# Optimization experiments

Hardware: AMD Instinct MI355X
Metric: run time of the kernel (lower is better)

The kernel has to match this reference:

```python
import jax, jax.numpy as jnp
import numpy as np

N = 100000      # nodes
E = 1600000     # edges (before self-loops)
F_IN = 16       # num_node_features
HID = 16        # hid
HEADS = 4       # in_head == out_head
B = 64          # num graphs
G = 16          # num_global_features
NEG_SLOPE = 0.2


def gat_conv(x, src, dst, W, a_src, a_dst, b, concat):
    """PyG-style GATConv. x:[N,F], W:[F,H*C], a_src/a_dst:[H,C], b:[H*C] or [C]."""
    n = x.shape[0]
    H, C = a_src.shape
    h = (x @ W).reshape(n, H, C)                       # [N,H,C]
    alpha_s = (h * a_src).sum(-1)                      # [N,H]
    alpha_d = (h * a_dst).sum(-1)                      # [N,H]
    e = jax.nn.leaky_relu(alpha_s[src] + alpha_d[dst], NEG_SLOPE)  # [E',H]
    # segment softmax over destination nodes (stable; max is grad-free)
    m = jax.lax.stop_gradient(jax.ops.segment_max(e, dst, num_segments=n))
    ex = jnp.exp(e - m[dst])
    denom = jax.ops.segment_sum(ex, dst, num_segments=n)
    alpha = ex / (denom[dst] + 1e-16)                  # [E',H]
    out = jax.ops.segment_sum(h[src] * alpha[:, :, None], dst, num_segments=n)  # [N,H,C]
    out = out.reshape(n, H * C) if concat else out.mean(axis=1)
    return out + b


def setup_inputs() -> dict:
    key = jax.random.key(0)
    ks = jax.random.split(key, 24)
    s = 0.1
    inp = {
        "x": jax.random.normal(ks[0], (N, F_IN), jnp.float32),
        "stats": jax.random.normal(ks[1], (B, G), jnp.float32),
        # conv1: F_IN -> HID, heads=HEADS, concat=True
        "W1": jax.random.normal(ks[2], (F_IN, HEADS * HID), jnp.float32) * s,
        "a1s": jax.random.normal(ks[3], (HEADS, HID), jnp.float32) * s,
        "a1d": jax.random.normal(ks[4], (HEADS, HID), jnp.float32) * s,
        "b1": jnp.zeros((HEADS * HID,), jnp.float32),
        # conv2: HID*HEADS -> HID, heads=HEADS, concat=False
        "W2": jax.random.normal(ks[5], (HEADS * HID, HEADS * HID), jnp.float32) * s,
        "a2s": jax.random.normal(ks[6], (HEADS, HID), jnp.float32) * s,
        "a2d": jax.random.normal(ks[7], (HEADS, HID), jnp.float32) * s,
        "b2": jnp.zeros((HID,), jnp.float32),
        # conv3: HID -> HID, heads=HEADS, concat=False
        "W3": jax.random.normal(ks[8], (HID, HEADS * HID), jnp.float32) * s,
        "a3s": jax.random.normal(ks[9], (HEADS, HID), jnp.float32) * s,
        "a3d": jax.random.normal(ks[10], (HEADS, HID), jnp.float32) * s,
        "b3": jnp.zeros((HID,), jnp.float32),
        # MLP head
        "fw1": jax.random.normal(ks[11], (HID + G, 32), jnp.float32) * s,
        "fb1": jnp.zeros((32,), jnp.float32),
        "fw2": jax.random.normal(ks[12], (32, 16), jnp.float32) * s,
        "fb2": jnp.zeros((16,), jnp.float32),
        "fw3": jax.random.normal(ks[13], (16, 1), jnp.float32) * s,
        "fb3": jnp.zeros((1,), jnp.float32),
        "edge_index": jax.random.randint(ks[14], (2, E), 0, N, jnp.int64),
        "batch": jnp.sort(jax.random.randint(ks[15], (N,), 0, B, jnp.int64)),
    }
    return inp


def reference(x, stats, W1, a1s, a1d, b1, W2, a2s, a2d, b2, W3, a3s, a3d, b3,
              fw1, fb1, fw2, fb2, fw3, fb3, edge_index, batch):
    n = x.shape[0]
    loops = jnp.arange(n, dtype=edge_index.dtype)
    src = jnp.concatenate([edge_index[0], loops])  # add_self_loops=True (PyG default)
    dst = jnp.concatenate([edge_index[1], loops])
    h = jax.nn.elu(gat_conv(x, src, dst, W1, a1s, a1d, b1, True))
    h = jax.nn.elu(gat_conv(h, src, dst, W2, a2s, a2d, b2, False))
    h = gat_conv(h, src, dst, W3, a3s, a3d, b3, False)
    nb = stats.shape[0]
    pooled = jax.ops.segment_sum(h, batch, num_segments=nb)
    counts = jax.ops.segment_sum(jnp.ones((n,), h.dtype), batch, num_segments=nb)
    pooled = pooled / jnp.maximum(counts, 1.0)[:, None]   # global_mean_pool
    z = jnp.concatenate([pooled, stats], axis=1)
    z = jax.nn.relu(z @ fw1 + fb1)
    z = jax.nn.relu(z @ fw2 + fb2)
    return z @ fw3 + fb3
```

## Files before the change

kernel.cpp:

```cpp
#include <hip/hip_runtime.h>
#include <hip/hip_bf16.h>
#include <hip/hip_fp16.h>

#define NNODES 100000
#define NEDGES 1600000
#define NB     64
#define NG     16
#define POOL_SLOTS (NB * NG + NB)

#define BKT_SHIFT 7
#define NPB 128
#define NBKT ((NNODES + NPB - 1) / NPB)
#define BCAP 4096
#define SCAT_BLOCKS 256
#define NL1_BLOCKS 2048

typedef float vf2 __attribute__((ext_vector_type(2)));

__device__ __forceinline__ float leaky02(float v) {
    return v > 0.0f ? v : 0.2f * v;
}

__device__ __forceinline__ unsigned char cvt_fp8(float a) {
    int r = __builtin_amdgcn_cvt_pk_fp8_f32(a, a, 0, false);
    return (unsigned char)(r & 0xFF);
}

__device__ __forceinline__ float4 loadQ4(const unsigned char* p) {
    int u = *(const int*)p;
    vf2 lo = __builtin_amdgcn_cvt_pk_f32_fp8(u, false);
    vf2 hi = __builtin_amdgcn_cvt_pk_f32_fp8(u, true);
    return make_float4(lo.x, lo.y, hi.x, hi.y);
}

__device__ __forceinline__ void storeH4(__half* p, float4 v) {
    __half2 a = __floats2half2_rn(v.x, v.y);
    __half2 b = __floats2half2_rn(v.z, v.w);
    uint2 raw;
    raw.x = *reinterpret_cast<unsigned*>(&a);
    raw.y = *reinterpret_cast<unsigned*>(&b);
    *(uint2*)p = raw;
}

template <int FIN>
__device__ __forceinline__ void nl_body_f32(const float* __restrict__ X,
                                            const float* __restrict__ W,
                                            const float* __restrict__ a_s,
                                            const float* __restrict__ a_d,
                                            unsigned char* __restrict__ H,
                                            float* __restrict__ AS,
                                            float* __restrict__ AD, int n,
                                            int wave0, int nwaves, int lane) {
    int head = lane >> 4;
    float w[FIN];
#pragma unroll
    for (int k = 0; k < FIN; ++k) w[k] = W[k * 64 + lane];
    float asl = a_s[lane], adl = a_d[lane];

    for (int i = wave0; i < n; i += nwaves) {
        const float* __restrict__ xr = X + (size_t)i * FIN;
        float acc = 0.0f;
#pragma unroll
        for (int k = 0; k < FIN; ++k) acc += xr[k] * w[k];
        H[(size_t)i * 64 + lane] = cvt_fp8(acc);
        float s1 = acc * asl, s2 = acc * adl;
#pragma unroll
        for (int off = 1; off < 16; off <<= 1) {
            s1 += __shfl_xor(s1, off);
            s2 += __shfl_xor(s2, off);
        }
        if ((lane & 15) == 0) {
            AS[(size_t)i * 4 + head] = s1;
            AD[(size_t)i * 4 + head] = s2;
        }
    }
}

template <int FIN>
__global__ void node_linear3h(const unsigned* __restrict__ X,
                              const float* __restrict__ W,
                              const float* __restrict__ a_s,
                              const float* __restrict__ a_d,
                              unsigned char* __restrict__ H,
                              float* __restrict__ AS,
                              float* __restrict__ AD, int n) {
    int lane = threadIdx.x & 63;
    int head = lane >> 4;
    int wave = __builtin_amdgcn_readfirstlane(
        (int)((blockIdx.x * blockDim.x + threadIdx.x) >> 6));
    int nwaves = (gridDim.x * blockDim.x) >> 6;

    float w[FIN];
#pragma unroll
    for (int k = 0; k < FIN; ++k) w[k] = W[k * 64 + lane];
    float asl = a_s[lane], adl = a_d[lane];

    for (int i = wave; i < n; i += nwaves) {
        const unsigned* __restrict__ xr = X + (size_t)i * (FIN / 2);
        float acc = 0.0f;
#pragma unroll
        for (int k = 0; k < FIN / 2; ++k) {
            unsigned u = xr[k];
            __half2 hh = *reinterpret_cast<const __half2*>(&u);
            float2 f = __half22float2(hh);
            acc += f.x * w[2 * k] + f.y * w[2 * k + 1];
        }
        H[(size_t)i * 64 + lane] = cvt_fp8(acc);
        float s1 = acc * asl, s2 = acc * adl;
#pragma unroll
        for (int off = 1; off < 16; off <<= 1) {
            s1 += __shfl_xor(s1, off);
            s2 += __shfl_xor(s2, off);
        }
        if ((lane & 15) == 0) {
            AS[(size_t)i * 4 + head] = s1;
            AD[(size_t)i * 4 + head] = s2;
        }
    }
}

__global__ void scatter_nl1(const int* __restrict__ src,
                            const int* __restrict__ dst,
                            int* __restrict__ bucketCnt,
                            unsigned int* __restrict__ pairs, int ne,
                            const float* __restrict__ X,
                            const float* __restrict__ W,
                            const float* __restrict__ a_s,
                            const float* __restrict__ a_d,
                            unsigned char* __restrict__ H,
                            float* __restrict__ AS,
                            float* __restrict__ AD, int n) {
    __shared__ int hist[NBKT];
    __shared__ int base[NBKT];
    int tid = threadIdx.x;

    if (blockIdx.x >= SCAT_BLOCKS) {
        int lane = tid & 63;
        int wave = __builtin_amdgcn_readfirstlane(
            (int)(((blockIdx.x - SCAT_BLOCKS) * blockDim.x + tid) >> 6));
        int nwaves = (NL1_BLOCKS * 256) >> 6;
        nl_body_f32<16>(X, W, a_s, a_d, H, AS, AD, n, wave, nwaves, lane);
        return;
    }

    for (int i = tid; i < NBKT; i += 256) hist[i] = 0;
    __syncthreads();

    int chunk = (ne + SCAT_BLOCKS - 1) / SCAT_BLOCKS;
    int beg = blockIdx.x * chunk;
    int end = min(beg + chunk, ne);

    for (int e0 = beg; e0 < end; e0 += 1024) {
        int d[4];
#pragma unroll
        for (int q = 0; q < 4; ++q) {
            int e = e0 + q * 256 + tid;
            d[q] = (e < end) ? __builtin_nontemporal_load(dst + e) : -1;
        }
#pragma unroll
        for (int q = 0; q < 4; ++q)
            if (d[q] >= 0) atomicAdd(&hist[d[q] >> BKT_SHIFT], 1);
    }
    __syncthreads();

    for (int i = tid; i < NBKT; i += 256) {
        int h = hist[i];
        base[i] = h ? atomicAdd(&bucketCnt[i], h) : 0;
        hist[i] = 0;
    }
    __syncthreads();

    for (int e0 = beg; e0 < end; e0 += 1024) {
        int d[4], s[4];
#pragma unroll
        for (int q = 0; q < 4; ++q) {
            int e = e0 + q * 256 + tid;
            d[q] = (e < end) ? __builtin_nontemporal_load(dst + e) : -1;
            s[q] = (e < end) ? __builtin_nontemporal_load(src + e) : 0;
        }
        int r[4], bkt[4];
#pragma unroll
        for (int q = 0; q < 4; ++q) {
            if (d[q] >= 0) {
                bkt[q] = d[q] >> BKT_SHIFT;
                r[q] = base[bkt[q]] + atomicAdd(&hist[bkt[q]], 1);
            }
        }
#pragma unroll
        for (int q = 0; q < 4; ++q) {
            if (d[q] >= 0 && r[q] < BCAP)
                __builtin_nontemporal_store(
                    (unsigned)s[q] | ((unsigned)(d[q] & (NPB - 1)) << 20),
                    pairs + (size_t)bkt[q] * BCAP + r[q]);
        }
    }
}

__global__ void bucket_sort(const unsigned int* __restrict__ pairs,
                            const int* __restrict__ bucketCnt,
                            int* __restrict__ srcs,
                            int* __restrict__ indptr, int n) {
    __shared__ int hist[NPB];
    __shared__ int offl[NPB];
    __shared__ int cur[NPB];
    __shared__ int red[256];
    __shared__ int lsrc[BCAP];
    int bkt = blockIdx.x;
    int t = threadIdx.x;
    int cnt = min(bucketCnt[bkt], BCAP);

    int partial = 0;
    for (int j = t; j < bkt; j += 256) partial += min(bucketCnt[j], BCAP);
    red[t] = partial;
    if (t < NPB) hist[t] = 0;
    __syncthreads();
    for (int s = 128; s > 0; s >>= 1) {
        if (t < s) red[t] += red[t + s];
        __syncthreads();
    }
    int boff = red[0];
    if (bkt == NBKT - 1 && t == 0) indptr[n] = boff + cnt;

    const unsigned int* __restrict__ p = pairs + (size_t)bkt * BCAP;
    unsigned int v[BCAP / 256];
#pragma unroll
    for (int i = 0; i < BCAP / 256; ++i) {
        int e = i * 256 + t;
        v[i] = 0u;
        if (e < cnt) {
            v[i] = __builtin_nontemporal_load(p + e);
            atomicAdd(&hist[v[i] >> 20], 1);
        }
    }
    __syncthreads();
    if (t < NPB) offl[t] = hist[t];
    __syncthreads();
    for (int off = 1; off < NPB; off <<= 1) {
        int x = 0;
        if (t < NPB && t >= off) x = offl[t - off];
        __syncthreads();
        if (t < NPB && t >= off) offl[t] += x;
        __syncthreads();
    }
    if (t < NPB) {
        int ex = offl[t] - hist[t];
        cur[t] = ex;
        int node = bkt * NPB + t;
        if (node < n) indptr[node] = boff + ex;
    }
    __syncthreads();
#pragma unroll
    for (int i = 0; i < BCAP / 256; ++i) {
        int e = i * 256 + t;
        if (e < cnt) {
            int r = atomicAdd(&cur[v[i] >> 20], 1);
            lsrc[r] = (int)(v[i] & 0xFFFFFu);
        }
    }
    __syncthreads();
    for (int e = t; e < cnt; e += 256) srcs[boff + e] = lsrc[e];
}

__device__ __forceinline__ float4 gat_agg_core(
    const unsigned char* __restrict__ H, const float* __restrict__ AS,
    const float* __restrict__ AD,
    const int* __restrict__ indptr, const int* __restrict__ srcs,
    int d, int grp, int sl, int head) {
    int beg = indptr[d], end = indptr[d + 1];
    int myS = 0;
    if (beg < end && sl < min(16, end - beg))
        myS = __builtin_nontemporal_load(srcs + beg + sl);

    float ad  = AD[(size_t)d * 4 + head];
    float asd = AS[(size_t)d * 4 + head];
    float t0 = asd + ad;
    float wself = __expf(leaky02(t0));
    float den = wself;
    float4 h4s = loadQ4(H + (size_t)d * 64 + sl * 4);
    float4 acc = make_float4(wself * h4s.x, wself * h4s.y,
                             wself * h4s.z, wself * h4s.w);

    for (int e0 = beg; e0 < end; e0 += 16) {
        int cnt = min(16, end - e0);
        int j = 0;
        for (; j + 8 <= cnt; j += 8) {
            int s[8]; float a[8]; float4 h4[8];
#pragma unroll
            for (int q = 0; q < 8; ++q)
                s[q] = __shfl(myS, (grp << 4) + j + q);
#pragma unroll
            for (int q = 0; q < 8; ++q)
                a[q] = AS[(size_t)s[q] * 4 + head];
#pragma unroll
            for (int q = 0; q < 8; ++q)
                h4[q] = loadQ4(H + (size_t)s[q] * 64 + sl * 4);
#pragma unroll
            for (int q = 0; q < 8; ++q) {
                float t = a[q] + ad;
                float w = __expf(leaky02(t));
                den += w;
                acc.x += w * h4[q].x; acc.y += w * h4[q].y;
                acc.z += w * h4[q].z; acc.w += w * h4[q].w;
            }
        }
        for (; j + 4 <= cnt; j += 4) {
            int s[4]; float a[4]; float4 h4[4];
#pragma unroll
            for (int q = 0; q < 4; ++q)
                s[q] = __shfl(myS, (grp << 4) + j + q);
#pragma unroll
            for (int q = 0; q < 4; ++q)
                a[q] = AS[(size_t)s[q] * 4 + head];
#pragma unroll
            for (int q = 0; q < 4; ++q)
                h4[q] = loadQ4(H + (size_t)s[q] * 64 + sl * 4);
#pragma unroll
            for (int q = 0; q < 4; ++q) {
                float t = a[q] + ad;
                float w = __expf(leaky02(t));
                den += w;
                acc.x += w * h4[q].x; acc.y += w * h4[q].y;
                acc.z += w * h4[q].z; acc.w += w * h4[q].w;
            }
        }
        for (; j < cnt; ++j) {
            int s = __shfl(myS, (grp << 4) + j);
            float t = AS[(size_t)s * 4 + head] + ad;
            float w = __expf(leaky02(t));
            float4 h4 = loadQ4(H + (size_t)s * 64 + sl * 4);
            den += w;
            acc.x += w * h4.x; acc.y += w * h4.y;
            acc.z += w * h4.z; acc.w += w * h4.w;
        }
        int nb = e0 + 16;
        if (nb < end && sl < min(16, end - nb))
            myS = __builtin_nontemporal_load(srcs + nb + sl);
    }
    float inv = 1.0f / (den + 1e-16f);
    return make_float4(acc.x * inv, acc.y * inv, acc.z * inv, acc.w * inv);
}

__global__ void gat_pull_l1(const unsigned char* __restrict__ H,
                            const float* __restrict__ AS,
                            const float* __restrict__ AD,
                            const int* __restrict__ indptr,
                            const int* __restrict__ srcs,
                            const float* __restrict__ bias,
                            __half* __restrict__ out, int n) {
    int lane = threadIdx.x & 63;
    int grp = lane >> 4, sl = lane & 15, head = sl >> 2;
    int wave = (blockIdx.x * blockDim.x + threadIdx.x) >> 6;
    int nwaves = (gridDim.x * blockDim.x) >> 6;
    for (int d0 = wave * 4; d0 < n; d0 += nwaves * 4) {
        int d = d0 + grp;
        if (d < n) {
            float4 v = gat_agg_core(H, AS, AD, indptr, srcs, d, grp, sl, head);
            float4 b4 = *(const float4*)(bias + sl * 4);
            v.x += b4.x; v.y += b4.y; v.z += b4.z; v.w += b4.w;
            v.x = v.x > 0.f ? v.x : __expf(v.x) - 1.f;
            v.y = v.y > 0.f ? v.y : __expf(v.y) - 1.f;
            v.z = v.z > 0.f ? v.z : __expf(v.z) - 1.f;
            v.w = v.w > 0.f ? v.w : __expf(v.w) - 1.f;
            storeH4(out + (size_t)d * 64 + sl * 4, v);
        }
    }
}

__global__ void gat_pull_l2(const unsigned char* __restrict__ H,
                            const float* __restrict__ AS,
                            float* __restrict__ AD,
                            const int* __restrict__ indptr,
                            const int* __restrict__ srcs,
                            const float* __restrict__ bias,
                            const float* __restrict__ W3,
                            const float* __restrict__ a3s,
                            const float* __restrict__ a3d,
                            unsigned char* __restrict__ Hout,
                            float* __restrict__ ASout, int n) {
    __shared__ float w3s[16 * 64];
    for (int i = threadIdx.x; i < 16 * 64; i += 256) w3s[i] = W3[i];
    __syncthreads();

    int lane = threadIdx.x & 63;
    int grp = lane >> 4, sl = lane & 15, head = sl >> 2;
    int wave = (blockIdx.x * blockDim.x + threadIdx.x) >> 6;
    int nwaves = (gridDim.x * blockDim.x) >> 6;
    float4 as4 = *(const float4*)(a3s + head * 16 + (sl & 3) * 4);
    float4 ad4 = *(const float4*)(a3d + head * 16 + (sl & 3) * 4);
    float4 b4  = *(const float4*)(bias + (sl & 3) * 4);

    for (int d0 = wave * 4; d0 < n; d0 += nwaves * 4) {
        int d = d0 + grp;
        if (d < n) {
            float4 v = gat_agg_core(H, AS, AD, indptr, srcs, d, grp, sl, head);
#pragma unroll
            for (int off = 4; off <= 8; off <<= 1) {
                v.x += __shfl_xor(v.x, off);
                v.y += __shfl_xor(v.y, off);
                v.z += __shfl_xor(v.z, off);
                v.w += __shfl_xor(v.w, off);
            }
            v.x = 0.25f * v.x + b4.x; v.y = 0.25f * v.y + b4.y;
            v.z = 0.25f * v.z + b4.z; v.w = 0.25f * v.w + b4.w;
            v.x = v.x > 0.f ? v.x : __expf(v.x) - 1.f;
            v.y = v.y > 0.f ? v.y : __expf(v.y) - 1.f;
            v.z = v.z > 0.f ? v.z : __expf(v.z) - 1.f;
            v.w = v.w > 0.f ? v.w : __expf(v.w) - 1.f;

            float xin[16];
#pragma unroll
            for (int q = 0; q < 4; ++q) {
                int srcl = (grp << 4) + q;
                xin[4 * q + 0] = __shfl(v.x, srcl);
                xin[4 * q + 1] = __shfl(v.y, srcl);
                xin[4 * q + 2] = __shfl(v.z, srcl);
                xin[4 * q + 3] = __shfl(v.w, srcl);
            }
            float4 o = make_float4(0.f, 0.f, 0.f, 0.f);
#pragma unroll
            for (int k = 0; k < 16; ++k) {
                float4 wr = *(const float4*)&w3s[k * 64 + 4 * sl];
                o.x += xin[k] * wr.x; o.y += xin[k] * wr.y;
                o.z += xin[k] * wr.z; o.w += xin[k] * wr.w;
            }
            int pk = __builtin_amdgcn_cvt_pk_fp8_f32(o.x, o.y, 0, false);
            pk = __builtin_amdgcn_cvt_pk_fp8_f32(o.z, o.w, pk, true);
            *(int*)(Hout + (size_t)d * 64 + 4 * sl) = pk;
            float s1 = o.x * as4.x + o.y * as4.y + o.z * as4.z + o.w * as4.w;
            float s2 = o.x * ad4.x + o.y * ad4.y + o.z * ad4.z + o.w * ad4.w;
            s1 += __shfl_xor(s1, 1); s1 += __shfl_xor(s1, 2);
            s2 += __shfl_xor(s2, 1); s2 += __shfl_xor(s2, 2);
            if ((sl & 3) == 0) {
                ASout[(size_t)d * 4 + head] = s1;
                AD[(size_t)d * 4 + head] = s2;
            }
        }
    }
}

__global__ void gat_pull_l3(const unsigned char* __restrict__ H,
                            const float* __restrict__ AS,
                            const float* __restrict__ AD,
                            const int* __restrict__ indptr,
                            const int* __restrict__ srcs,
                            const float* __restrict__ bias,
                            const int* __restrict__ batch,
                            float* __restrict__ PC, int n) {
    __shared__ float lp[POOL_SLOTS];
    for (int i = threadIdx.x; i < POOL_SLOTS; i += 256) lp[i] = 0.f;
    __syncthreads();

    int lane = threadIdx.x & 63;
    int grp = lane >> 4, sl = lane & 15, head = sl >> 2;
    int wave = (blockIdx.x * blockDim.x + threadIdx.x) >> 6;
    int nwaves = (gridDim.x * blockDim.x) >> 6;
    float4 b4 = *(const float4*)(bias + (sl & 3) * 4);

    for (int d0 = wave * 4; d0 < n; d0 += nwaves * 4) {
        int d = d0 + grp;
        if (d < n) {
            float4 v = gat_agg_core(H, AS, AD, indptr, srcs, d, grp, sl, head);
#pragma unroll
            for (int off = 4; off <= 8; off <<= 1) {
                v.x += __shfl_xor(v.x, off);
                v.y += __shfl_xor(v.y, off);
                v.z += __shfl_xor(v.z, off);
                v.w += __shfl_xor(v.w, off);
            }
            v.x = 0.25f * v.x + b4.x; v.y = 0.25f * v.y + b4.y;
            v.z = 0.25f * v.z + b4.z; v.w = 0.25f * v.w + b4.w;
            if (sl < 4) {
                int b = batch[d];
                atomicAdd(&lp[b * 16 + sl * 4 + 0], v.x);
                atomicAdd(&lp[b * 16 + sl * 4 + 1], v.y);
                atomicAdd(&lp[b * 16 + sl * 4 + 2], v.z);
                atomicAdd(&lp[b * 16 + sl * 4 + 3], v.w);
                if (sl == 0) atomicAdd(&lp[NB * NG + b], 1.0f);
            }
        }
    }
    __syncthreads();
    for (int i = threadIdx.x; i < POOL_SLOTS; i += 256) {
        float s = lp[i];
        if (s != 0.f) atomicAdd(&PC[i], s);
    }
}

__global__ void mlp_head(const float* __restrict__ pooled_counts,
                         const float* __restrict__ stats,
                         const float* __restrict__ fw1, const float* __restrict__ fb1,
                         const float* __restrict__ fw2, const float* __restrict__ fb2,
                         const float* __restrict__ fw3, const float* __restrict__ fb3,
                         float* __restrict__ out) {
    int g = threadIdx.x;
    if (g >= NB) return;
    const float* pooled = pooled_counts;
    const float* counts = pooled_counts + NB * NG;
    float z[32];
    float inv = 1.0f / fmaxf(counts[g], 1.0f);
#pragma unroll
    for (int c = 0; c < 16; ++c) z[c] = pooled[g * 16 + c] * inv;
#pragma unroll
    for (int c = 0; c < 16; ++c) z[16 + c] = stats[g * 16 + c];

    float z1[32];
#pragma unroll
    for (int j = 0; j < 32; ++j) {
        float acc = fb1[j];
        for (int k = 0; k < 32; ++k) acc += z[k] * fw1[k * 32 + j];
        z1[j] = fmaxf(acc, 0.0f);
    }
    float z2[16];
#pragma unroll
    for (int j = 0; j < 16; ++j) {
        float acc = fb2[j];
        for (int k = 0; k < 32; ++k) acc += z1[k] * fw2[k * 16 + j];
        z2[j] = fmaxf(acc, 0.0f);
    }
    float acc = fb3[0];
#pragma unroll
    for (int k = 0; k < 16; ++k) acc += z2[k] * fw3[k];
    out[g] = acc;
}

extern "C" void kernel_launch(void* const* d_in, const int* in_sizes, int n_in,
                              void* d_out, int out_size, void* d_ws, size_t ws_size,
                              hipStream_t stream) {
    const float* x    = (const float*)d_in[0];
    const float* stats= (const float*)d_in[1];
    const float* W1   = (const float*)d_in[2];
    const float* a1s  = (const float*)d_in[3];
    const float* a1d  = (const float*)d_in[4];
    const float* b1   = (const float*)d_in[5];
    const float* W2   = (const float*)d_in[6];
    const float* a2s  = (const float*)d_in[7];
    const float* a2d  = (const float*)d_in[8];
    const float* b2   = (const float*)d_in[9];
    const float* W3   = (const float*)d_in[10];
    const float* a3s  = (const float*)d_in[11];
    const float* a3d  = (const float*)d_in[12];
    const float* b3   = (const float*)d_in[13];
    const float* fw1  = (const float*)d_in[14];
    const float* fb1  = (const float*)d_in[15];
    const float* fw2  = (const float*)d_in[16];
    const float* fb2  = (const float*)d_in[17];
    const float* fw3  = (const float*)d_in[18];
    const float* fb3  = (const float*)d_in[19];
    const int* ei     = (const int*)d_in[20];
    const int* batch  = (const int*)d_in[21];

    const int n = NNODES, ne = NEDGES;
    const int* srcI = ei;
    const int* dstI = ei + ne;

    unsigned char* HqA = (unsigned char*)d_ws;
    unsigned char* HqB = HqA + (size_t)n * 64;
    float* ASa  = (float*)(HqB + (size_t)n * 64);
    float* ASb  = ASa + (size_t)n * 4;
    float* AD   = ASb + (size_t)n * 4;
    float* PC   = AD + (size_t)n * 4;
    int* bucketCnt = (int*)(PC + POOL_SLOTS);
    int* indptr    = bucketCnt + NBKT;
    int* srcs      = indptr + (n + 1);
    size_t off = (size_t)((char*)(srcs + ne) - (char*)d_ws);
    off = (off + 255) & ~(size_t)255;
    unsigned int* pairs = (unsigned int*)((char*)d_ws + off);
    __half* B16 = (__half*)pairs;

    const int TB = 256;
    const int nlBlocks   = 2048;
    const int pullBlocks = (n + 15) / 16;

    hipMemsetAsync(PC, 0, (POOL_SLOTS + NBKT) * sizeof(int), stream);

    scatter_nl1<<<SCAT_BLOCKS + NL1_BLOCKS, TB, 0, stream>>>(
        srcI, dstI, bucketCnt, pairs, ne,
        x, W1, a1s, a1d, HqA, ASa, AD, n);
    bucket_sort<<<NBKT, TB, 0, stream>>>(pairs, bucketCnt, srcs, indptr, n);

    gat_pull_l1<<<pullBlocks, TB, 0, stream>>>(HqA, ASa, AD, indptr, srcs, b1,
                                               B16, n);

    node_linear3h<64><<<nlBlocks, TB, 0, stream>>>((const unsigned*)B16, W2,
                                                   a2s, a2d, HqA, ASa, AD, n);
    gat_pull_l2<<<pullBlocks, TB, 0, stream>>>(HqA, ASa, AD, indptr, srcs, b2,
                                               W3, a3s, a3d, HqB, ASb, n);
    gat_pull_l3<<<pullBlocks, TB, 0, stream>>>(HqB, ASb, AD, indptr, srcs, b3,
                                               batch, PC, n);

    mlp_head<<<1, 64, 0, stream>>>(PC, stats, fw1, fb1, fw2, fb2, fw3, fb3,
                                   (float*)d_out);
}
```

Before: 395.9 us.

## Aggregate raw 16-dim inputs before linear transform in layers 1 and 3

Uses linearity of attention aggregation: instead of gathering 64-wide transformed features per edge, layers 1 and 3 gather the 16-wide pre-transform features (fp8) and apply W after aggregation, per head. Attention logits are computed from folded W·a vectors. This cuts per-edge gather bytes by a factor of four for two of the three layers, at the cost of a per-node 16x64 matmul after aggregation and some extra shuffles. Non-temporal loads in the scatter kernel are also replaced with plain loads.

```diff
diff --git a/kernel.cpp b/kernel.cpp
--- a/kernel.cpp
+++ b/kernel.cpp
@@ -20,19 +20,28 @@
 __device__ __forceinline__ float leaky02(float v) {
     return v > 0.0f ? v : 0.2f * v;
 }
-
+__device__ __forceinline__ float elu1(float v) {
+    return v > 0.0f ? v : __expf(v) - 1.0f;
+}
+__device__ __forceinline__ float dot4(float4 a, float4 b) {
+    return a.x * b.x + a.y * b.y + a.z * b.z + a.w * b.w;
+}
+
+__device__ __forceinline__ int packQ4(float4 v) {
+    int pk = __builtin_amdgcn_cvt_pk_fp8_f32(v.x, v.y, 0, false);
+    pk = __builtin_amdgcn_cvt_pk_fp8_f32(v.z, v.w, pk, true);
+    return pk;
+}
 __device__ __forceinline__ unsigned char cvt_fp8(float a) {
     int r = __builtin_amdgcn_cvt_pk_fp8_f32(a, a, 0, false);
     return (unsigned char)(r & 0xFF);
 }
-
 __device__ __forceinline__ float4 loadQ4(const unsigned char* p) {
     int u = *(const int*)p;
     vf2 lo = __builtin_amdgcn_cvt_pk_f32_fp8(u, false);
     vf2 hi = __builtin_amdgcn_cvt_pk_f32_fp8(u, true);
     return make_float4(lo.x, lo.y, hi.x, hi.y);
 }
-
 __device__ __forceinline__ void storeH4(__half* p, float4 v) {
     __half2 a = __floats2half2_rn(v.x, v.y);
     __half2 b = __floats2half2_rn(v.z, v.w);
@@ -42,36 +51,336 @@
     *(uint2*)p = raw;
 }
 
-template <int FIN>
-__device__ __forceinline__ void nl_body_f32(const float* __restrict__ X,
-                                            const float* __restrict__ W,
-                                            const float* __restrict__ a_s,
-                                            const float* __restrict__ a_d,
-                                            unsigned char* __restrict__ H,
-                                            float* __restrict__ AS,
-                                            float* __restrict__ AD, int n,
-                                            int wave0, int nwaves, int lane) {
-    int head = lane >> 4;
-    float w[FIN];
-#pragma unroll
-    for (int k = 0; k < FIN; ++k) w[k] = W[k * 64 + lane];
-    float asl = a_s[lane], adl = a_d[lane];
-
-    for (int i = wave0; i < n; i += nwaves) {
-        const float* __restrict__ xr = X + (size_t)i * FIN;
-        float acc = 0.0f;
-#pragma unroll
-        for (int k = 0; k < FIN; ++k) acc += xr[k] * w[k];
-        H[(size_t)i * 64 + lane] = cvt_fp8(acc);
-        float s1 = acc * asl, s2 = acc * adl;
-#pragma unroll
-        for (int off = 1; off < 16; off <<= 1) {
-            s1 += __shfl_xor(s1, off);
-            s2 += __shfl_xor(s2, off);
-        }
-        if ((lane & 15) == 0) {
-            AS[(size_t)i * 4 + head] = s1;
-            AD[(size_t)i * 4 + head] = s2;
+__device__ __forceinline__ void nl1_body(const float* __restrict__ X,
+                                         const float* __restrict__ W1,
+                                         const float* __restrict__ a1s,
+                                         const float* __restrict__ a1d,
+                                         unsigned char* __restrict__ Xq,
+                                         float* __restrict__ AS,
+                                         float* __restrict__ AD, int n,
+                                         int quad0, int nquads, int q) {
+    float ws[4][4], wd[4][4];
+#pragma unroll
+    for (int h = 0; h < 4; ++h)
+#pragma unroll
+        for (int j = 0; j < 4; ++j) {
+            float s = 0.f, d = 0.f;
+            for (int c = 0; c < 16; ++c) {
+                float wv = W1[(4 * q + j) * 64 + h * 16 + c];
+                s += wv * a1s[h * 16 + c];
+                d += wv * a1d[h * 16 + c];
+            }
+            ws[h][j] = s; wd[h][j] = d;
+        }
+
+    for (int i = quad0; i < n; i += nquads) {
+        float4 x4 = *(const float4*)(X + (size_t)i * 16 + 4 * q);
+        *(int*)(Xq + (size_t)i * 16 + 4 * q) = packQ4(x4);
+        float s[4], d[4];
+#pragma unroll
+        for (int h = 0; h < 4; ++h) {
+            s[h] = x4.x * ws[h][0] + x4.y * ws[h][1] + x4.z * ws[h][2] + x4.w * ws[h][3];
+            d[h] = x4.x * wd[h][0] + x4.y * wd[h][1] + x4.z * wd[h][2] + x4.w * wd[h][3];
+        }
+#pragma unroll
+        for (int h = 0; h < 4; ++h) {
+            s[h] += __shfl_xor(s[h], 1); s[h] += __shfl_xor(s[h], 2);
+            d[h] += __shfl_xor(d[h], 1); d[h] += __shfl_xor(d[h], 2);
+        }
+        if (q == 0) *(float4*)(AS + (size_t)i * 4) = make_float4(s[0], s[1], s[2], s[3]);
+        if (q == 1) *(float4*)(AD + (size_t)i * 4) = make_float4(d[0], d[1], d[2], d[3]);
+    }
+}
+
+__global__ void scatter_nl1(const int* __restrict__ src,
+                            const int* __restrict__ dst,
+                            int* __restrict__ bucketCnt,
+                            unsigned int* __restrict__ pairs, int ne,
+                            const float* __restrict__ X,
+                            const float* __restrict__ W1,
+                            const float* __restrict__ a1s,
+                            const float* __restrict__ a1d,
+                            unsigned char* __restrict__ Xq,
+                            float* __restrict__ AS,
+                            float* __restrict__ AD, int n) {
+    __shared__ int hist[NBKT];
+    __shared__ int base[NBKT];
+    int tid = threadIdx.x;
+
+    if (blockIdx.x >= SCAT_BLOCKS) {
+        int q = tid & 3;
+        int quad0 = ((blockIdx.x - SCAT_BLOCKS) * 256 + tid) >> 2;
+        int nquads = (NL1_BLOCKS * 256) >> 2;
+        nl1_body(X, W1, a1s, a1d, Xq, AS, AD, n, quad0, nquads, q);
+        return;
+    }
+
+    for (int i = tid; i < NBKT; i += 256) hist[i] = 0;
+    __syncthreads();
+
+    int chunk = (ne + SCAT_BLOCKS - 1) / SCAT_BLOCKS;
+    int beg = blockIdx.x * chunk;
+    int end = min(beg + chunk, ne);
+
+    for (int e0 = beg; e0 < end; e0 += 1024) {
+        int d[4];
+#pragma unroll
+        for (int q = 0; q < 4; ++q) {
+            int e = e0 + q * 256 + tid;
+            d[q] = (e < end) ? dst[e] : -1;
+        }
+#pragma unroll
+        for (int q = 0; q < 4; ++q)
+            if (d[q] >= 0) atomicAdd(&hist[d[q] >> BKT_SHIFT], 1);
+    }
+    __syncthreads();
+
+    for (int i = tid; i < NBKT; i += 256) {
+        int h = hist[i];
+        base[i] = h ? atomicAdd(&bucketCnt[i], h) : 0;
+        hist[i] = 0;
+    }
+    __syncthreads();
+
+    for (int e0 = beg; e0 < end; e0 += 1024) {
+        int d[4], s[4];
+#pragma unroll
+        for (int q = 0; q < 4; ++q) {
+            int e = e0 + q * 256 + tid;
+            d[q] = (e < end) ? dst[e] : -1;
+            s[q] = (e < end) ? src[e] : 0;
+        }
+        int r[4], bkt[4];
+#pragma unroll
+        for (int q = 0; q < 4; ++q) {
+            if (d[q] >= 0) {
+                bkt[q] = d[q] >> BKT_SHIFT;
+                r[q] = base[bkt[q]] + atomicAdd(&hist[bkt[q]], 1);
+            }
+        }
+#pragma unroll
+        for (int q = 0; q < 4; ++q) {
+            if (d[q] >= 0 && r[q] < BCAP)
+                pairs[(size_t)bkt[q] * BCAP + r[q]] =
+                    (unsigned)s[q] | ((unsigned)(d[q] & (NPB - 1)) << 20);
+        }
+    }
+}
+
+__global__ void bucket_sort(const unsigned int* __restrict__ pairs,
+                            const int* __restrict__ bucketCnt,
+                            int* __restrict__ srcs,
+                            int* __restrict__ indptr, int n) {
+    __shared__ int hist[NPB];
+    __shared__ int offl[NPB];
+    __shared__ int cur[NPB];
+    __shared__ int red[256];
+    __shared__ int lsrc[BCAP];
+    int bkt = blockIdx.x;
+    int t = threadIdx.x;
+    int cnt = min(bucketCnt[bkt], BCAP);
+
+    int partial = 0;
+    for (int j = t; j < bkt; j += 256) partial += min(bucketCnt[j], BCAP);
+    red[t] = partial;
+    if (t < NPB) hist[t] = 0;
+    __syncthreads();
+    for (int s = 128; s > 0; s >>= 1) {
+        if (t < s) red[t] += red[t + s];
+        __syncthreads();
+    }
+    int boff = red[0];
+    if (bkt == NBKT - 1 && t == 0) indptr[n] = boff + cnt;
+
+    const unsigned int* __restrict__ p = pairs + (size_t)bkt * BCAP;
+    unsigned int v[BCAP / 256];
+#pragma unroll
+    for (int i = 0; i < BCAP / 256; ++i) {
+        int e = i * 256 + t;
+        v[i] = 0u;
+        if (e < cnt) {
+            v[i] = p[e];
+            atomicAdd(&hist[v[i] >> 20], 1);
+        }
+    }
+    __syncthreads();
+    if (t < NPB) offl[t] = hist[t];
+    __syncthreads();
+    for (int off = 1; off < NPB; off <<= 1) {
+        int x = 0;
+        if (t < NPB && t >= off) x = offl[t - off];
+        __syncthreads();
+        if (t < NPB && t >= off) offl[t] += x;
+        __syncthreads();
+    }
+    if (t < NPB) {
+        int ex = offl[t] - hist[t];
+        cur[t] = ex;
+        int node = bkt * NPB + t;
+        if (node < n) indptr[node] = boff + ex;
+    }
+    __syncthreads();
+#pragma unroll
+    for (int i = 0; i < BCAP / 256; ++i) {
+        int e = i * 256 + t;
+        if (e < cnt) {
+            int r = atomicAdd(&cur[v[i] >> 20], 1);
+            lsrc[r] = (int)(v[i] & 0xFFFFFu);
+        }
+    }
+    __syncthreads();
+    for (int e = t; e < cnt; e += 256) srcs[boff + e] = lsrc[e];
+}
+
+__device__ __forceinline__ float4 gat_agg16(
+    const unsigned char* __restrict__ Xq, const float* __restrict__ AS,
+    const float* __restrict__ AD,
+    const int* __restrict__ indptr, const int* __restrict__ srcs,
+    int d, int grp, int sl, int head, int dq, float& denOut) {
+    float ad  = AD[(size_t)d * 4 + head];
+    float asd = AS[(size_t)d * 4 + head];
+    float t0 = asd + ad;
+    float wself = __expf(leaky02(t0));
+    float den = wself;
+    float4 x4s = loadQ4(Xq + (size_t)d * 16 + dq * 4);
+    float4 acc = make_float4(wself * x4s.x, wself * x4s.y,
+                             wself * x4s.z, wself * x4s.w);
+
+    int beg = indptr[d], end = indptr[d + 1];
+    for (int e0 = beg; e0 < end; e0 += 16) {
+        int cnt = min(16, end - e0);
+        int myS = (sl < cnt) ? srcs[e0 + sl] : 0;
+        int j = 0;
+        for (; j + 4 <= cnt; j += 4) {
+            int s[4]; float a[4]; float4 h4[4];
+#pragma unroll
+            for (int q = 0; q < 4; ++q)
+                s[q] = __shfl(myS, (grp << 4) + j + q);
+#pragma unroll
+            for (int q = 0; q < 4; ++q)
+                a[q] = AS[(size_t)s[q] * 4 + head];
+#pragma unroll
+            for (int q = 0; q < 4; ++q)
+                h4[q] = loadQ4(Xq + (size_t)s[q] * 16 + dq * 4);
+#pragma unroll
+            for (int q = 0; q < 4; ++q) {
+                float t = a[q] + ad;
+                float w = __expf(leaky02(t));
+                den += w;
+                acc.x += w * h4[q].x; acc.y += w * h4[q].y;
+                acc.z += w * h4[q].z; acc.w += w * h4[q].w;
+            }
+        }
+        for (; j < cnt; ++j) {
+            int s = __shfl(myS, (grp << 4) + j);
+            float t = AS[(size_t)s * 4 + head] + ad;
+            float w = __expf(leaky02(t));
+            float4 h4 = loadQ4(Xq + (size_t)s * 16 + dq * 4);
+            den += w;
+            acc.x += w * h4.x; acc.y += w * h4.y;
+            acc.z += w * h4.z; acc.w += w * h4.w;
+        }
+    }
+    denOut = den;
+    return acc;
+}
+
+__device__ __forceinline__ float4 gat_agg64(
+    const unsigned char* __restrict__ H, const float* __restrict__ AS,
+    const float* __restrict__ AD,
+    const int* __restrict__ indptr, const int* __restrict__ srcs,
+    int d, int grp, int sl, int head, float& denOut) {
+    float ad  = AD[(size_t)d * 4 + head];
+    float asd = AS[(size_t)d * 4 + head];
+    float t0 = asd + ad;
+    float wself = __expf(leaky02(t0));
+    float den = wself;
+    float4 h4s = loadQ4(H + (size_t)d * 64 + sl * 4);
+    float4 acc = make_float4(wself * h4s.x, wself * h4s.y,
+                             wself * h4s.z, wself * h4s.w);
+
+    int beg = indptr[d], end = indptr[d + 1];
+    for (int e0 = beg; e0 < end; e0 += 16) {
+        int cnt = min(16, end - e0);
+        int myS = (sl < cnt) ? srcs[e0 + sl] : 0;
+        int j = 0;
+        for (; j + 4 <= cnt; j += 4) {
+            int s[4]; float a[4]; float4 h4[4];
+#pragma unroll
+            for (int q = 0; q < 4; ++q)
+                s[q] = __shfl(myS, (grp << 4) + j + q);
+#pragma unroll
+            for (int q = 0; q < 4; ++q)
+                a[q] = AS[(size_t)s[q] * 4 + head];
+#pragma unroll
+            for (int q = 0; q < 4; ++q)
+                h4[q] = loadQ4(H + (size_t)s[q] * 64 + sl * 4);
+#pragma unroll
+            for (int q = 0; q < 4; ++q) {
+                float t = a[q] + ad;
+                float w = __expf(leaky02(t));
+                den += w;
+                acc.x += w * h4[q].x; acc.y += w * h4[q].y;
+                acc.z += w * h4[q].z; acc.w += w * h4[q].w;
+            }
+        }
+        for (; j < cnt; ++j) {
+            int s = __shfl(myS, (grp << 4) + j);
+            float t = AS[(size_t)s * 4 + head] + ad;
+            float w = __expf(leaky02(t));
+            float4 h4 = loadQ4(H + (size_t)s * 64 + sl * 4);
+            den += w;
+            acc.x += w * h4.x; acc.y += w * h4.y;
+            acc.z += w * h4.z; acc.w += w * h4.w;
+        }
+    }
+    denOut = den;
+    return acc;
+}
+
+__global__ void gat_pull_l1(const unsigned char* __restrict__ Xq,
+                            const float* __restrict__ AS,
+                            const float* __restrict__ AD,
+                            const int* __restrict__ indptr,
+                            const int* __restrict__ srcs,
+                            const float* __restrict__ W1,
+                            const float* __restrict__ bias,
+                            __half* __restrict__ out, int n) {
+    __shared__ float wlds[16 * 64];
+    for (int i = threadIdx.x; i < 16 * 64; i += 256) wlds[i] = W1[i];
+    __syncthreads();
+
+    int lane = threadIdx.x & 63;
+    int grp = lane >> 4, sl = lane & 15, head = sl >> 2, dq = sl & 3;
+    int wave = (blockIdx.x * blockDim.x + threadIdx.x) >> 6;
+    int nwaves = (gridDim.x * blockDim.x) >> 6;
+    for (int d0 = wave * 4; d0 < n; d0 += nwaves * 4) {
+        int d = d0 + grp;
+        if (d < n) {
+            float den;
+            float4 acc = gat_agg16(Xq, AS, AD, indptr, srcs, d, grp, sl, head, dq, den);
+            float inv = 1.0f / (den + 1e-16f);
+            float4 v = make_float4(acc.x * inv, acc.y * inv, acc.z * inv, acc.w * inv);
+            float xin[16];
+#pragma unroll
+            for (int q = 0; q < 4; ++q) {
+                int srcl = (grp << 4) + head * 4 + q;
+                xin[4 * q + 0] = __shfl(v.x, srcl);
+                xin[4 * q + 1] = __shfl(v.y, srcl);
+                xin[4 * q + 2] = __shfl(v.z, srcl);
+                xin[4 * q + 3] = __shfl(v.w, srcl);
+            }
+            float4 o = make_float4(0.f, 0.f, 0.f, 0.f);
+#pragma unroll
+            for (int k = 0; k < 16; ++k) {
+                float4 wr = *(const float4*)&wlds[k * 64 + 4 * sl];
+                o.x += xin[k] * wr.x; o.y += xin[k] * wr.y;
+                o.z += xin[k] * wr.z; o.w += xin[k] * wr.w;
+            }
+            float4 b4 = *(const float4*)(bias + 4 * sl);
+            o.x = elu1(o.x + b4.x); o.y = elu1(o.y + b4.y);
+            o.z = elu1(o.z + b4.z); o.w = elu1(o.w + b4.w);
+            storeH4(out + (size_t)d * 64 + sl * 4, o);
         }
     }
 }
@@ -119,253 +428,6 @@
     }
 }
 
-__global__ void scatter_nl1(const int* __restrict__ src,
-                            const int* __restrict__ dst,
-                            int* __restrict__ bucketCnt,
-                            unsigned int* __restrict__ pairs, int ne,
-                            const float* __restrict__ X,
-                            const float* __restrict__ W,
-                            const float* __restrict__ a_s,
-                            const float* __restrict__ a_d,
-                            unsigned char* __restrict__ H,
-                            float* __restrict__ AS,
-                            float* __restrict__ AD, int n) {
-    __shared__ int hist[NBKT];
-    __shared__ int base[NBKT];
-    int tid = threadIdx.x;
-
-    if (blockIdx.x >= SCAT_BLOCKS) {
-        int lane = tid & 63;
-        int wave = __builtin_amdgcn_readfirstlane(
-            (int)(((blockIdx.x - SCAT_BLOCKS) * blockDim.x + tid) >> 6));
-        int nwaves = (NL1_BLOCKS * 256) >> 6;
-        nl_body_f32<16>(X, W, a_s, a_d, H, AS, AD, n, wave, nwaves, lane);
-        return;
-    }
-
-    for (int i = tid; i < NBKT; i += 256) hist[i] = 0;
-    __syncthreads();
-
-    int chunk = (ne + SCAT_BLOCKS - 1) / SCAT_BLOCKS;
-    int beg = blockIdx.x * chunk;
-    int end = min(beg + chunk, ne);
-
-    for (int e0 = beg; e0 < end; e0 += 1024) {
-        int d[4];
-#pragma unroll
-        for (int q = 0; q < 4; ++q) {
-            int e = e0 + q * 256 + tid;
-            d[q] = (e < end) ? __builtin_nontemporal_load(dst + e) : -1;
-        }
-#pragma unroll
-        for (int q = 0; q < 4; ++q)
-            if (d[q] >= 0) atomicAdd(&hist[d[q] >> BKT_SHIFT], 1);
-    }
-    __syncthreads();
-
-    for (int i = tid; i < NBKT; i += 256) {
-        int h = hist[i];
-        base[i] = h ? atomicAdd(&bucketCnt[i], h) : 0;
-        hist[i] = 0;
-    }
-    __syncthreads();
-
-    for (int e0 = beg; e0 < end; e0 += 1024) {
-        int d[4], s[4];
-#pragma unroll
-        for (int q = 0; q < 4; ++q) {
-            int e = e0 + q * 256 + tid;
-            d[q] = (e < end) ? __builtin_nontemporal_load(dst + e) : -1;
-            s[q] = (e < end) ? __builtin_nontemporal_load(src + e) : 0;
-        }
-        int r[4], bkt[4];
-#pragma unroll
-        for (int q = 0; q < 4; ++q) {
-            if (d[q] >= 0) {
-                bkt[q] = d[q] >> BKT_SHIFT;
-                r[q] = base[bkt[q]] + atomicAdd(&hist[bkt[q]], 1);
-            }
-        }
-#pragma unroll
-        for (int q = 0; q < 4; ++q) {
-            if (d[q] >= 0 && r[q] < BCAP)
-                __builtin_nontemporal_store(
-                    (unsigned)s[q] | ((unsigned)(d[q] & (NPB - 1)) << 20),
-                    pairs + (size_t)bkt[q] * BCAP + r[q]);
-        }
-    }
-}
-
-__global__ void bucket_sort(const unsigned int* __restrict__ pairs,
-                            const int* __restrict__ bucketCnt,
-                            int* __restrict__ srcs,
-                            int* __restrict__ indptr, int n) {
-    __shared__ int hist[NPB];
-    __shared__ int offl[NPB];
-    __shared__ int cur[NPB];
-    __shared__ int red[256];
-    __shared__ int lsrc[BCAP];
-    int bkt = blockIdx.x;
-    int t = threadIdx.x;
-    int cnt = min(bucketCnt[bkt], BCAP);
-
-    int partial = 0;
-    for (int j = t; j < bkt; j += 256) partial += min(bucketCnt[j], BCAP);
-    red[t] = partial;
-    if (t < NPB) hist[t] = 0;
-    __syncthreads();
-    for (int s = 128; s > 0; s >>= 1) {
-        if (t < s) red[t] += red[t + s];
-        __syncthreads();
-    }
-    int boff = red[0];
-    if (bkt == NBKT - 1 && t == 0) indptr[n] = boff + cnt;
-
-    const unsigned int* __restrict__ p = pairs + (size_t)bkt * BCAP;
-    unsigned int v[BCAP / 256];
-#pragma unroll
-    for (int i = 0; i < BCAP / 256; ++i) {
-        int e = i * 256 + t;
-        v[i] = 0u;
-        if (e < cnt) {
-            v[i] = __builtin_nontemporal_load(p + e);
-            atomicAdd(&hist[v[i] >> 20], 1);
-        }
-    }
-    __syncthreads();
-    if (t < NPB) offl[t] = hist[t];
-    __syncthreads();
-    for (int off = 1; off < NPB; off <<= 1) {
-        int x = 0;
-        if (t < NPB && t >= off) x = offl[t - off];
-        __syncthreads();
-        if (t < NPB && t >= off) offl[t] += x;
-        __syncthreads();
-    }
-    if (t < NPB) {
-        int ex = offl[t] - hist[t];
-        cur[t] = ex;
-        int node = bkt * NPB + t;
-        if (node < n) indptr[node] = boff + ex;
-    }
-    __syncthreads();
-#pragma unroll
-    for (int i = 0; i < BCAP / 256; ++i) {
-        int e = i * 256 + t;
-        if (e < cnt) {
-            int r = atomicAdd(&cur[v[i] >> 20], 1);
-            lsrc[r] = (int)(v[i] & 0xFFFFFu);
-        }
-    }
-    __syncthreads();
-    for (int e = t; e < cnt; e += 256) srcs[boff + e] = lsrc[e];
-}
-
-__device__ __forceinline__ float4 gat_agg_core(
-    const unsigned char* __restrict__ H, const float* __restrict__ AS,
-    const float* __restrict__ AD,
-    const int* __restrict__ indptr, const int* __restrict__ srcs,
-    int d, int grp, int sl, int head) {
-    int beg = indptr[d], end = indptr[d + 1];
-    int myS = 0;
-    if (beg < end && sl < min(16, end - beg))
-        myS = __builtin_nontemporal_load(srcs + beg + sl);
-
-    float ad  = AD[(size_t)d * 4 + head];
-    float asd = AS[(size_t)d * 4 + head];
-    float t0 = asd + ad;
-    float wself = __expf(leaky02(t0));
-    float den = wself;
-    float4 h4s = loadQ4(H + (size_t)d * 64 + sl * 4);
-    float4 acc = make_float4(wself * h4s.x, wself * h4s.y,
-                             wself * h4s.z, wself * h4s.w);
-
-    for (int e0 = beg; e0 < end; e0 += 16) {
-        int cnt = min(16, end - e0);
-        int j = 0;
-        for (; j + 8 <= cnt; j += 8) {
-            int s[8]; float a[8]; float4 h4[8];
-#pragma unroll
-            for (int q = 0; q < 8; ++q)
-                s[q] = __shfl(myS, (grp << 4) + j + q);
-#pragma unroll
-            for (int q = 0; q < 8; ++q)
-                a[q] = AS[(size_t)s[q] * 4 + head];
-#pragma unroll
-            for (int q = 0; q < 8; ++q)
-                h4[q] = loadQ4(H + (size_t)s[q] * 64 + sl * 4);
-#pragma unroll
-            for (int q = 0; q < 8; ++q) {
-                float t = a[q] + ad;
-                float w = __expf(leaky02(t));
-                den += w;
-                acc.x += w * h4[q].x; acc.y += w * h4[q].y;
-                acc.z += w * h4[q].z; acc.w += w * h4[q].w;
-            }
-        }
-        for (; j + 4 <= cnt; j += 4) {
-            int s[4]; float a[4]; float4 h4[4];
-#pragma unroll
-            for (int q = 0; q < 4; ++q)
-                s[q] = __shfl(myS, (grp << 4) + j + q);
-#pragma unroll
-            for (int q = 0; q < 4; ++q)
-                a[q] = AS[(size_t)s[q] * 4 + head];
-#pragma unroll
-            for (int q = 0; q < 4; ++q)
-                h4[q] = loadQ4(H + (size_t)s[q] * 64 + sl * 4);
-#pragma unroll
-            for (int q = 0; q < 4; ++q) {
-                float t = a[q] + ad;
-                float w = __expf(leaky02(t));
-                den += w;
-                acc.x += w * h4[q].x; acc.y += w * h4[q].y;
-                acc.z += w * h4[q].z; acc.w += w * h4[q].w;
-            }
-        }
-        for (; j < cnt; ++j) {
-            int s = __shfl(myS, (grp << 4) + j);
-            float t = AS[(size_t)s * 4 + head] + ad;
-            float w = __expf(leaky02(t));
-            float4 h4 = loadQ4(H + (size_t)s * 64 + sl * 4);
-            den += w;
-            acc.x += w * h4.x; acc.y += w * h4.y;
-            acc.z += w * h4.z; acc.w += w * h4.w;
-        }
-        int nb = e0 + 16;
-        if (nb < end && sl < min(16, end - nb))
-            myS = __builtin_nontemporal_load(srcs + nb + sl);
-    }
-    float inv = 1.0f / (den + 1e-16f);
-    return make_float4(acc.x * inv, acc.y * inv, acc.z * inv, acc.w * inv);
-}
-
-__global__ void gat_pull_l1(const unsigned char* __restrict__ H,
-                            const float* __restrict__ AS,
-                            const float* __restrict__ AD,
-                            const int* __restrict__ indptr,
-                            const int* __restrict__ srcs,
-                            const float* __restrict__ bias,
-                            __half* __restrict__ out, int n) {
-    int lane = threadIdx.x & 63;
-    int grp = lane >> 4, sl = lane & 15, head = sl >> 2;
-    int wave = (blockIdx.x * blockDim.x + threadIdx.x) >> 6;
-    int nwaves = (gridDim.x * blockDim.x) >> 6;
-    for (int d0 = wave * 4; d0 < n; d0 += nwaves * 4) {
-        int d = d0 + grp;
-        if (d < n) {
-            float4 v = gat_agg_core(H, AS, AD, indptr, srcs, d, grp, sl, head);
-            float4 b4 = *(const float4*)(bias + sl * 4);
-            v.x += b4.x; v.y += b4.y; v.z += b4.z; v.w += b4.w;
-            v.x = v.x > 0.f ? v.x : __expf(v.x) - 1.f;
-            v.y = v.y > 0.f ? v.y : __expf(v.y) - 1.f;
-            v.z = v.z > 0.f ? v.z : __expf(v.z) - 1.f;
-            v.w = v.w > 0.f ? v.w : __expf(v.w) - 1.f;
-            storeH4(out + (size_t)d * 64 + sl * 4, v);
-        }
-    }
-}
-
 __global__ void gat_pull_l2(const unsigned char* __restrict__ H,
                             const float* __restrict__ AS,
                             float* __restrict__ AD,
@@ -375,24 +437,32 @@
                             const float* __restrict__ W3,
                             const float* __restrict__ a3s,
                             const float* __restrict__ a3d,
-                            unsigned char* __restrict__ Hout,
-                            float* __restrict__ ASout, int n) {
-    __shared__ float w3s[16 * 64];
-    for (int i = threadIdx.x; i < 16 * 64; i += 256) w3s[i] = W3[i];
-    __syncthreads();
-
+                            unsigned char* __restrict__ Xq3,
+                            float* __restrict__ AS3, int n) {
     int lane = threadIdx.x & 63;
-    int grp = lane >> 4, sl = lane & 15, head = sl >> 2;
+    int grp = lane >> 4, sl = lane & 15, head = sl >> 2, dq = sl & 3;
     int wave = (blockIdx.x * blockDim.x + threadIdx.x) >> 6;
     int nwaves = (gridDim.x * blockDim.x) >> 6;
-    float4 as4 = *(const float4*)(a3s + head * 16 + (sl & 3) * 4);
-    float4 ad4 = *(const float4*)(a3d + head * 16 + (sl & 3) * 4);
-    float4 b4  = *(const float4*)(bias + (sl & 3) * 4);
+
+    float4 w3s4 = make_float4(0, 0, 0, 0), w3d4 = make_float4(0, 0, 0, 0);
+    for (int c = 0; c < 16; ++c) {
+        float as_ = a3s[head * 16 + c], ad_ = a3d[head * 16 + c];
+        float w0 = W3[(4 * dq + 0) * 64 + head * 16 + c];
+        float w1 = W3[(4 * dq + 1) * 64 + head * 16 + c];
+        float w2 = W3[(4 * dq + 2) * 64 + head * 16 + c];
+        float w3 = W3[(4 * dq + 3) * 64 + head * 16 + c];
+        w3s4.x += w0 * as_; w3s4.y += w1 * as_; w3s4.z += w2 * as_; w3s4.w += w3 * as_;
+        w3d4.x += w0 * ad_; w3d4.y += w1 * ad_; w3d4.z += w2 * ad_; w3d4.w += w3 * ad_;
+    }
+    float4 b4 = *(const float4*)(bias + dq * 4);
 
     for (int d0 = wave * 4; d0 < n; d0 += nwaves * 4) {
         int d = d0 + grp;
         if (d < n) {
-            float4 v = gat_agg_core(H, AS, AD, indptr, srcs, d, grp, sl, head);
+            float den;
+            float4 acc = gat_agg64(H, AS, AD, indptr, srcs, d, grp, sl, head, den);
+            float inv = 1.0f / (den + 1e-16f);
+            float4 v = make_float4(acc.x * inv, acc.y * inv, acc.z * inv, acc.w * inv);
 #pragma unroll
             for (int off = 4; off <= 8; off <<= 1) {
                 v.x += __shfl_xor(v.x, off);
@@ -400,17 +470,56 @@
                 v.z += __shfl_xor(v.z, off);
                 v.w += __shfl_xor(v.w, off);
             }
-            v.x = 0.25f * v.x + b4.x; v.y = 0.25f * v.y + b4.y;
-            v.z = 0.25f * v.z + b4.z; v.w = 0.25f * v.w + b4.w;
-            v.x = v.x > 0.f ? v.x : __expf(v.x) - 1.f;
-            v.y = v.y > 0.f ? v.y : __expf(v.y) - 1.f;
-            v.z = v.z > 0.f ? v.z : __expf(v.z) - 1.f;
-            v.w = v.w > 0.f ? v.w : __expf(v.w) - 1.f;
-
+            v.x = elu1(0.25f * v.x + b4.x);
+            v.y = elu1(0.25f * v.y + b4.y);
+            v.z = elu1(0.25f * v.z + b4.z);
+            v.w = elu1(0.25f * v.w + b4.w);
+            if (sl < 4)
+                *(int*)(Xq3 + (size_t)d * 16 + 4 * sl) = packQ4(v);
+            float s1 = dot4(v, w3s4);
+            float s2 = dot4(v, w3d4);
+            s1 += __shfl_xor(s1, 1); s1 += __shfl_xor(s1, 2);
+            s2 += __shfl_xor(s2, 1); s2 += __shfl_xor(s2, 2);
+            if (dq == 0) {
+                AS3[(size_t)d * 4 + head] = s1;
+                AD[(size_t)d * 4 + head] = s2;
+            }
+        }
+    }
+}
+
+__global__ void gat_pull_l3(const unsigned char* __restrict__ Xq,
+                            const float* __restrict__ AS,
+                            const float* __restrict__ AD,
+                            const int* __restrict__ indptr,
+                            const int* __restrict__ srcs,
+                            const float* __restrict__ W3,
+                            const float* __restrict__ bias,
+                            const int* __restrict__ batch,
+                            float* __restrict__ PC, int n) {
+    __shared__ float wlds[16 * 64];
+    __shared__ float lp[POOL_SLOTS];
+    for (int i = threadIdx.x; i < 16 * 64; i += 256) wlds[i] = W3[i];
+    for (int i = threadIdx.x; i < POOL_SLOTS; i += 256) lp[i] = 0.f;
+    __syncthreads();
+
+    int lane = threadIdx.x & 63;
+    int grp = lane >> 4, sl = lane & 15, head = sl >> 2, dq = sl & 3;
+    int wave = (blockIdx.x * blockDim.x + threadIdx.x) >> 6;
+    int nwaves = (gridDim.x * blockDim.x) >> 6;
+    float4 b4 = *(const float4*)(bias + dq * 4);
+
+    for (int d0 = wave * 4; d0 < n; d0 += nwaves * 4) {
+        int d = d0 + grp;
+        if (d < n) {
+            float den;
+            float4 acc = gat_agg16(Xq, AS, AD, indptr, srcs, d, grp, sl, head, dq, den);
+            float inv = 1.0f / (den + 1e-16f);
+            float4 v = make_float4(acc.x * inv, acc.y * inv, acc.z * inv, acc.w * inv);
             float xin[16];
 #pragma unroll
             for (int q = 0; q < 4; ++q) {
-                int srcl = (grp << 4) + q;
+                int srcl = (grp << 4) + head * 4 + q;
                 xin[4 * q + 0] = __shfl(v.x, srcl);
                 xin[4 * q + 1] = __shfl(v.y, srcl);
                 xin[4 * q + 2] = __shfl(v.z, srcl);
@@ -419,62 +528,25 @@
             float4 o = make_float4(0.f, 0.f, 0.f, 0.f);
 #pragma unroll
             for (int k = 0; k < 16; ++k) {
-                float4 wr = *(const float4*)&w3s[k * 64 + 4 * sl];
+                float4 wr = *(const float4*)&wlds[k * 64 + head * 16 + dq * 4];
                 o.x += xin[k] * wr.x; o.y += xin[k] * wr.y;
                 o.z += xin[k] * wr.z; o.w += xin[k] * wr.w;
             }
-            int pk = __builtin_amdgcn_cvt_pk_fp8_f32(o.x, o.y, 0, false);
-            pk = __builtin_amdgcn_cvt_pk_fp8_f32(o.z, o.w, pk, true);
-            *(int*)(Hout + (size_t)d * 64 + 4 * sl) = pk;
-            float s1 = o.x * as4.x + o.y * as4.y + o.z * as4.z + o.w * as4.w;
-            float s2 = o.x * ad4.x + o.y * ad4.y + o.z * ad4.z + o.w * ad4.w;
-            s1 += __shfl_xor(s1, 1); s1 += __shfl_xor(s1, 2);
-            s2 += __shfl_xor(s2, 1); s2 += __shfl_xor(s2, 2);
-            if ((sl & 3) == 0) {
-                ASout[(size_t)d * 4 + head] = s1;
-                AD[(size_t)d * 4 + head] = s2;
-            }
-        }
-    }
-}
-
-__global__ void gat_pull_l3(const unsigned char* __restrict__ H,
-                            const float* __restrict__ AS,
-                            const float* __restrict__ AD,
-                            const int* __restrict__ indptr,
-                            const int* __restrict__ srcs,
-                            const float* __restrict__ bias,
-                            const int* __restrict__ batch,
-                            float* __restrict__ PC, int n) {
-    __shared__ float lp[POOL_SLOTS];
-    for (int i = threadIdx.x; i < POOL_SLOTS; i += 256) lp[i] = 0.f;
-    __syncthreads();
-
-    int lane = threadIdx.x & 63;
-    int grp = lane >> 4, sl = lane & 15, head = sl >> 2;
-    int wave = (blockIdx.x * blockDim.x + threadIdx.x) >> 6;
-    int nwaves = (gridDim.x * blockDim.x) >> 6;
-    float4 b4 = *(const float4*)(bias + (sl & 3) * 4);
-
-    for (int d0 = wave * 4; d0 < n; d0 += nwaves * 4) {
-        int d = d0 + grp;
-        if (d < n) {
-            float4 v = gat_agg_core(H, AS, AD, indptr, srcs, d, grp, sl, head);
 #pragma unroll
             for (int off = 4; off <= 8; off <<= 1) {
-                v.x += __shfl_xor(v.x, off);
-                v.y += __shfl_xor(v.y, off);
-                v.z += __shfl_xor(v.z, off);
-                v.w += __shfl_xor(v.w, off);
-            }
-            v.x = 0.25f * v.x + b4.x; v.y = 0.25f * v.y + b4.y;
-            v.z = 0.25f * v.z + b4.z; v.w = 0.25f * v.w + b4.w;
+                o.x += __shfl_xor(o.x, off);
+                o.y += __shfl_xor(o.y, off);
+                o.z += __shfl_xor(o.z, off);
+                o.w += __shfl_xor(o.w, off);
+            }
+            o.x = 0.25f * o.x + b4.x; o.y = 0.25f * o.y + b4.y;
+            o.z = 0.25f * o.z + b4.z; o.w = 0.25f * o.w + b4.w;
             if (sl < 4) {
                 int b = batch[d];
-                atomicAdd(&lp[b * 16 + sl * 4 + 0], v.x);
-                atomicAdd(&lp[b * 16 + sl * 4 + 1], v.y);
-                atomicAdd(&lp[b * 16 + sl * 4 + 2], v.z);
-                atomicAdd(&lp[b * 16 + sl * 4 + 3], v.w);
+                atomicAdd(&lp[b * 16 + sl * 4 + 0], o.x);
+                atomicAdd(&lp[b * 16 + sl * 4 + 1], o.y);
+                atomicAdd(&lp[b * 16 + sl * 4 + 2], o.z);
+                atomicAdd(&lp[b * 16 + sl * 4 + 3], o.w);
                 if (sl == 0) atomicAdd(&lp[NB * NG + b], 1.0f);
             }
         }
@@ -553,9 +625,9 @@
     const int* srcI = ei;
     const int* dstI = ei + ne;
 
-    unsigned char* HqA = (unsigned char*)d_ws;
-    unsigned char* HqB = HqA + (size_t)n * 64;
-    float* ASa  = (float*)(HqB + (size_t)n * 64);
+    unsigned char* Xq = (unsigned char*)d_ws;
+    unsigned char* Hq2 = Xq + (size_t)n * 16;
+    float* ASa  = (float*)(Hq2 + (size_t)n * 64);
     float* ASb  = ASa + (size_t)n * 4;
     float* AD   = ASb + (size_t)n * 4;
     float* PC   = AD + (size_t)n * 4;
@@ -575,18 +647,18 @@
 
     scatter_nl1<<<SCAT_BLOCKS + NL1_BLOCKS, TB, 0, stream>>>(
         srcI, dstI, bucketCnt, pairs, ne,
-        x, W1, a1s, a1d, HqA, ASa, AD, n);
+        x, W1, a1s, a1d, Xq, ASa, AD, n);
     bucket_sort<<<NBKT, TB, 0, stream>>>(pairs, bucketCnt, srcs, indptr, n);
 
-    gat_pull_l1<<<pullBlocks, TB, 0, stream>>>(HqA, ASa, AD, indptr, srcs, b1,
-                                               B16, n);
+    gat_pull_l1<<<pullBlocks, TB, 0, stream>>>(Xq, ASa, AD, indptr, srcs,
+                                               W1, b1, B16, n);
 
     node_linear3h<64><<<nlBlocks, TB, 0, stream>>>((const unsigned*)B16, W2,
-                                                   a2s, a2d, HqA, ASa, AD, n);
-    gat_pull_l2<<<pullBlocks, TB, 0, stream>>>(HqA, ASa, AD, indptr, srcs, b2,
-                                               W3, a3s, a3d, HqB, ASb, n);
-    gat_pull_l3<<<pullBlocks, TB, 0, stream>>>(HqB, ASb, AD, indptr, srcs, b3,
-                                               batch, PC, n);
+                                                   a2s, a2d, Hq2, ASb, AD, n);
+    gat_pull_l2<<<pullBlocks, TB, 0, stream>>>(Hq2, ASb, AD, indptr, srcs, b2,
+                                               W3, a3s, a3d, Xq, ASa, n);
+    gat_pull_l3<<<pullBlocks, TB, 0, stream>>>(Xq, ASa, AD, indptr, srcs,
+                                               W3, b3, batch, PC, n);
 
     mlp_head<<<1, 64, 0, stream>>>(PC, stats, fw1, fb1, fw2, fb2, fw3, fb3,
                                    (float*)d_out);
```

Result: no change. 393.9 us (-0.5%).
